# Optimization experiments

Hardware: AMD Instinct MI355X
Metric: run time of the kernel (lower is better)

## Reference

```python
import jax, jax.numpy as jnp
import numpy as np

S = 7          # number of slots
B = 8192       # batch
D = 1024       # input_dim
E = 256        # slot_embedding_dim
H = 512        # rnn_hidden_dim
SH = 256       # slot_hidden_dim
V = 100        # labels per slot (uniform)


def _lstm_cell(x, h, c, W_ih, W_hh, b_ih, b_hh):
    # PyTorch LSTMCell: gates ordered i, f, g, o
    gates = x @ W_ih.T + b_ih + h @ W_hh.T + b_hh
    i, f, g, o = jnp.split(gates, 4, axis=-1)
    i = jax.nn.sigmoid(i); f = jax.nn.sigmoid(f)
    g = jnp.tanh(g); o = jax.nn.sigmoid(o)
    c_new = f * c + i * g
    h_new = o * jnp.tanh(c_new)
    return h_new, c_new


def setup_inputs() -> dict:
    key = jax.random.key(0)
    ks = jax.random.split(key, 24)
    sc = 0.05
    D0 = D + E  # layer-0 input size
    inp = {
        'inputs': jax.random.normal(ks[0], (B, D), jnp.float32),
        'labels': jax.random.randint(ks[1], (S - 1, B), 0, V),
        'start': jax.random.normal(ks[2], (E,), jnp.float32),
        'emb': jax.random.normal(ks[3], (S - 1, V, E), jnp.float32) * sc,
        # layer 0 (input size D0)
        'W_ih0': jax.random.normal(ks[4], (S, 4 * H, D0), jnp.float32) * sc,
        'W_hh0': jax.random.normal(ks[5], (S, 4 * H, H), jnp.float32) * sc,
        'b_ih0': jax.random.normal(ks[6], (S, 4 * H), jnp.float32) * sc,
        'b_hh0': jax.random.normal(ks[7], (S, 4 * H), jnp.float32) * sc,
        'hwN_W0': jax.random.normal(ks[8], (S, H, D0 + H), jnp.float32) * sc,
        'hwN_b0': jax.random.normal(ks[9], (S, H), jnp.float32) * sc,
        'hwL_W0': jax.random.normal(ks[10], (S, H, D0), jnp.float32) * sc,
        # layer 1 (input size H)
        'W_ih1': jax.random.normal(ks[11], (S, 4 * H, H), jnp.float32) * sc,
        'W_hh1': jax.random.normal(ks[12], (S, 4 * H, H), jnp.float32) * sc,
        'b_ih1': jax.random.normal(ks[13], (S, 4 * H), jnp.float32) * sc,
        'b_hh1': jax.random.normal(ks[14], (S, 4 * H), jnp.float32) * sc,
        'hwN_W1': jax.random.normal(ks[15], (S, H, H + H), jnp.float32) * sc,
        'hwN_b1': jax.random.normal(ks[16], (S, H), jnp.float32) * sc,
        'hwL_W1': jax.random.normal(ks[17], (S, H, H), jnp.float32) * sc,
        # slot hidden + classifier
        'sh_W': jax.random.normal(ks[18], (S, SH, H), jnp.float32) * sc,
        'sh_b': jax.random.normal(ks[19], (S, SH), jnp.float32) * sc,
        'pred_W': jax.random.normal(ks[20], (S, V, SH), jnp.float32) * sc,
        'pred_b': jax.random.normal(ks[21], (S, V), jnp.float32) * sc,
    }
    return inp


def reference(inputs, labels, start, emb,
              W_ih0, W_hh0, b_ih0, b_hh0, hwN_W0, hwN_b0, hwL_W0,
              W_ih1, W_hh1, b_ih1, b_hh1, hwN_W1, hwN_b1, hwL_W1,
              sh_W, sh_b, pred_W, pred_b):
    bsz = inputs.shape[0]
    cur_emb = jnp.broadcast_to(start[None, :], (bsz, E))
    h0 = jnp.zeros((bsz, H), inputs.dtype); c0 = jnp.zeros((bsz, H), inputs.dtype)
    h1 = jnp.zeros((bsz, H), inputs.dtype); c1 = jnp.zeros((bsz, H), inputs.dtype)
    logits_all = []
    for i in range(S):  # slots are a short, structurally distinct recurrence
        x = jnp.concatenate([inputs, cur_emb], axis=-1)  # [B, D+E]
        # layer 0
        h0, c0 = _lstm_cell(x, h0, c0, W_ih0[i], W_hh0[i], b_ih0[i], b_hh0[i])
        gate = jax.nn.sigmoid(jnp.concatenate([x, h0], -1) @ hwN_W0[i].T + hwN_b0[i])
        cur = gate * h0 + (1.0 - gate) * (x @ hwL_W0[i].T)
        # layer 1
        h1, c1 = _lstm_cell(cur, h1, c1, W_ih1[i], W_hh1[i], b_ih1[i], b_hh1[i])
        gate1 = jax.nn.sigmoid(jnp.concatenate([cur, h1], -1) @ hwN_W1[i].T + hwN_b1[i])
        # (highway output of last layer feeds nothing further for this slot)
        _ = gate1 * h1 + (1.0 - gate1) * (cur @ hwL_W1[i].T)
        hidden = jax.nn.relu(h1 @ sh_W[i].T + sh_b[i])     # [B, SH]
        logits_all.append(hidden @ pred_W[i].T + pred_b[i])  # [B, V]
        if i < S - 1:
            cur_emb = emb[i][labels[i]]  # teacher-forced embedding lookup
    return jnp.stack(logits_all, axis=0)  # [S, B, V]
```

## Files before the change

### kernel.cpp

```cpp
#include <hip/hip_runtime.h>

#define SLOTS 7
#define BATCH 8192

typedef __attribute__((ext_vector_type(8))) __bf16 bf16x8;
typedef __attribute__((ext_vector_type(4))) float f32x4;

__device__ __forceinline__ void gl_lds16(const __bf16* g, __bf16* l) {
  __builtin_amdgcn_global_load_lds(
      (const __attribute__((address_space(1))) void*)g,
      (__attribute__((address_space(3))) void*)l, 16, 0, 0);
}

__device__ __forceinline__ float sigmoidf_(float x) {
  return 1.f / (1.f + __expf(-x));
}
__device__ __forceinline__ float tanhf_(float x) {
  float xc = fminf(fmaxf(x, -15.f), 15.f);
  float e = __expf(2.f * xc);
  return (e - 1.f) / (e + 1.f);
}

#define VMW(n) asm volatile("s_waitcnt vmcnt(" #n ")" ::: "memory")
#define BARF()                       \
  __builtin_amdgcn_s_barrier();      \
  asm volatile("" ::: "memory")

__global__ void __launch_bounds__(512, 2)
gemm8p(const __bf16* __restrict__ A, int lda,
       const __bf16* __restrict__ Bw, int ldb,
       const float* __restrict__ b_ih, const float* __restrict__ b_hh,
       float* __restrict__ cst, __bf16* __restrict__ hout, int hld, int hoff,
       int N, int NT) {
  extern __shared__ __bf16 lds[];
#define LDSH(b, s) (lds + (((b) << 2) + (s)) * 8192)
  const int tid = threadIdx.x;
  const int w = tid >> 6, lane = tid & 63;
  const int wr = w >> 2, wc = w & 3;
  const int ln = lane & 15, lh = lane >> 4;
  const int nbx = N >> 8;
  const int NB = gridDim.x;
  const int bid = blockIdx.x;
  const int wg = (bid & 7) * (NB >> 3) + (bid >> 3);
  const int bx = wg % nbx, by = wg / nbx;
  const int blockM = by << 8, blockN = bx << 8;

  f32x4 acc[8][4];
#pragma unroll
  for (int i = 0; i < 8; ++i)
#pragma unroll
    for (int j = 0; j < 4; ++j) acc[i][j] = (f32x4){0.f, 0.f, 0.f, 0.f};

  auto stage = [&](int nb, int s, int kt) {
    const __bf16* base = (s & 1) ? Bw : A;
    const int ld = (s & 1) ? ldb : lda;
    const int rb = (s & 1) ? blockN : blockM;
    const int kh = s >> 1;
#pragma unroll
    for (int j = 0; j < 2; ++j) {
      const int c = j * 512 + w * 64 + lane;
      const int row = c >> 2;
      const int blklog = (c & 3) ^ ((c >> 3) & 3);
      const __bf16* src =
          base + (size_t)(rb + row) * ld + kt * 64 + kh * 32 + blklog * 8;
      gl_lds16(src, LDSH(nb, s) + j * 4096 + w * 512);
    }
  };

  bf16x8 a[8], b0[2], b1[2];
  const int swz = ((lh ^ ((ln >> 1) & 3)) << 3);

#define RDA(slot)                                                            \
  {                                                                          \
    const __bf16* ap = LDSH(buf, slot);                                      \
    _Pragma("unroll") for (int mi = 0; mi < 8; ++mi) a[mi] =                 \
        *(const bf16x8*)&ap[(wr * 128 + mi * 16 + ln) * 32 + swz];           \
  }
#define RDB(slot)                                                            \
  {                                                                          \
    const __bf16* bp = LDSH(buf, slot);                                      \
    _Pragma("unroll") for (int ni = 0; ni < 2; ++ni) {                       \
      b0[ni] = *(const bf16x8*)&bp[(wc * 64 + ni * 16 + ln) * 32 + swz];     \
      b1[ni] = *(const bf16x8*)&bp[(wc * 64 + 32 + ni * 16 + ln) * 32 + swz];\
    }                                                                        \
  }
#define MFMAC(bp, nh)                                                        \
  __builtin_amdgcn_s_setprio(1);                                             \
  _Pragma("unroll") for (int mi = 0; mi < 8; ++mi)                           \
      _Pragma("unroll") for (int ni = 0; ni < 2; ++ni)                       \
          acc[mi][(nh)*2 + ni] = __builtin_amdgcn_mfma_f32_16x16x32_bf16(    \
              a[mi], bp[ni], acc[mi][(nh)*2 + ni], 0, 0, 0);                 \
  __builtin_amdgcn_s_setprio(0);

#pragma unroll
  for (int s4 = 0; s4 < 4; ++s4) stage(0, s4, 0);
  VMW(0);
  BARF();

  int buf = 0;
  for (int t = 0; t < NT; ++t) {
    const int nb = buf ^ 1;
    const bool hn = (t + 1 < NT);
    RDA(0); RDB(1);
    if (hn) { stage(nb, 0, t + 1); stage(nb, 1, t + 1); }
    MFMAC(b0, 0); MFMAC(b1, 1);
    RDA(2); RDB(3);
    if (hn) { stage(nb, 2, t + 1); stage(nb, 3, t + 1); }
    MFMAC(b0, 0); MFMAC(b1, 1);
    VMW(0);
    BARF();
    buf = nb;
  }
#undef RDA
#undef RDB
#undef MFMAC
#undef LDSH

  const int row0 = blockM + wr * 128 + (lh << 2);
  const int h = (((blockN >> 6) + wc) << 4) + ln;
  const float bs0 = b_ih[h] + b_hh[h];
  const float bs1 = b_ih[512 + h] + b_hh[512 + h];
  const float bs2 = b_ih[1024 + h] + b_hh[1024 + h];
  const float bs3 = b_ih[1536 + h] + b_hh[1536 + h];
#pragma unroll
  for (int mi = 0; mi < 8; ++mi)
#pragma unroll
    for (int r = 0; r < 4; ++r) {
      const int row = row0 + mi * 16 + r;
      float gi = sigmoidf_(acc[mi][0][r] + bs0);
      float gf = sigmoidf_(acc[mi][1][r] + bs1);
      float gg = tanhf_(acc[mi][2][r] + bs2);
      float go = sigmoidf_(acc[mi][3][r] + bs3);
      const size_t ci = (size_t)row * 512 + h;
      float cn = gf * cst[ci] + gi * gg;
      cst[ci] = cn;
      hout[(size_t)row * hld + hoff + h] = (__bf16)(go * tanhf_(cn));
    }
}

template <int MODE>
__global__ void __launch_bounds__(256)
gemm_bt(const __bf16* __restrict__ A, int lda,
        const __bf16* __restrict__ Bw, int ldb,
        void* __restrict__ Cout, int ldc,
        const float* __restrict__ bias,
        const float* __restrict__ auxr,
        __bf16* __restrict__ hout, int hld, int hoff,
        const __bf16* __restrict__ hsrc,
        int M, int N, int K, int Nreal) {
  __shared__ __align__(16) __bf16 As[2][128 * 32];
  __shared__ __align__(16) __bf16 Bs[2][128 * 32];
  const int w = threadIdx.x >> 6;
  const int lane = threadIdx.x & 63;
  const int wr = w >> 1, wc = w & 1;
  const int rowBase = blockIdx.y << 7;
  const int colBase = blockIdx.x << 7;
  const int sr = lane >> 2;
  const int sc = (lane & 3) << 3;

  f32x4 acc[4][4];
#pragma unroll
  for (int i = 0; i < 4; ++i)
#pragma unroll
    for (int j = 0; j < 4; ++j) acc[i][j] = (f32x4){0.f, 0.f, 0.f, 0.f};

  const int nsteps = K >> 5;

#define STAGE(bi, k0)                                                           \
  {                                                                             \
    const __bf16* ga = A + (size_t)(rowBase + (w << 5) + sr) * lda + (k0) + sc; \
    gl_lds16(ga, &As[(bi)][(w << 5) * 32]);                                     \
    gl_lds16(ga + (size_t)16 * lda, &As[(bi)][((w << 5) + 16) * 32]);           \
    const __bf16* gb = Bw + (size_t)(colBase + (w << 5) + sr) * ldb + (k0) + sc;\
    gl_lds16(gb, &Bs[(bi)][(w << 5) * 32]);                                     \
    gl_lds16(gb + (size_t)16 * ldb, &Bs[(bi)][((w << 5) + 16) * 32]);           \
  }

  STAGE(0, 0);
  __syncthreads();
  int buf = 0;
  const int ln = lane & 15;
  const int kg = (lane >> 4) << 3;
  for (int t = 0; t < nsteps; ++t) {
    if (t + 1 < nsteps) STAGE(buf ^ 1, (t + 1) << 5);
    bf16x8 av[4], bv[4];
#pragma unroll
    for (int i = 0; i < 4; ++i)
      av[i] = *(const bf16x8*)&As[buf][((wr << 6) + (i << 4) + ln) * 32 + kg];
#pragma unroll
    for (int i = 0; i < 4; ++i)
      bv[i] = *(const bf16x8*)&Bs[buf][((wc << 6) + (i << 4) + ln) * 32 + kg];
#pragma unroll
    for (int mi = 0; mi < 4; ++mi)
#pragma unroll
      for (int ni = 0; ni < 4; ++ni)
        acc[mi][ni] = __builtin_amdgcn_mfma_f32_16x16x32_bf16(
            av[mi], bv[ni], acc[mi][ni], 0, 0, 0);
    __syncthreads();
    buf ^= 1;
  }
#undef STAGE

  const int lh = lane >> 4;
  const int row0 = rowBase + (wr << 6) + (lh << 2);
  const int col0 = colBase + (wc << 6) + ln;

  if (MODE == 0) {
    float* C = (float*)Cout;
#pragma unroll
    for (int mi = 0; mi < 4; ++mi)
#pragma unroll
      for (int ni = 0; ni < 4; ++ni) {
        const int col = col0 + (ni << 4);
#pragma unroll
        for (int r = 0; r < 4; ++r)
          C[(size_t)(row0 + (mi << 4) + r) * ldc + col] = acc[mi][ni][r];
      }
  } else if (MODE == 1) {
    __bf16* C = (__bf16*)Cout;
#pragma unroll
    for (int mi = 0; mi < 4; ++mi)
#pragma unroll
      for (int ni = 0; ni < 4; ++ni) {
        const int col = col0 + (ni << 4);
        const float b = bias[col];
#pragma unroll
        for (int r = 0; r < 4; ++r) {
          float v = fmaxf(acc[mi][ni][r] + b, 0.f);
          C[(size_t)(row0 + (mi << 4) + r) * ldc + col] = (__bf16)v;
        }
      }
  } else if (MODE == 2) {
    float* C = (float*)Cout;
#pragma unroll
    for (int mi = 0; mi < 4; ++mi)
#pragma unroll
      for (int ni = 0; ni < 4; ++ni) {
        const int col = col0 + (ni << 4);
        if (col < Nreal) {
          const float b = bias[col];
#pragma unroll
          for (int r = 0; r < 4; ++r)
            C[(size_t)(row0 + (mi << 4) + r) * ldc + col] = acc[mi][ni][r] + b;
        }
      }
  } else if (MODE == 6) {
    __bf16* C = (__bf16*)Cout;
#pragma unroll
    for (int mi = 0; mi < 4; ++mi)
#pragma unroll
      for (int ni = 0; ni < 4; ++ni) {
        const int col = col0 + (ni << 4);
#pragma unroll
        for (int r = 0; r < 4; ++r) {
          const int row = row0 + (mi << 4) + r;
          float xp = auxr[(size_t)row * 1024 + col];
          float hwl = auxr[(size_t)row * 1024 + 512 + col];
          float gn = sigmoidf_(acc[mi][ni][r] + xp + bias[col]);
          float hn = (float)hsrc[(size_t)row * 512 + col];
          C[(size_t)row * ldc + col] = (__bf16)(gn * hn + (1.f - gn) * hwl);
          hout[(size_t)row * hld + hoff + col] = (__bf16)hn;
        }
      }
  }
}

__global__ void pack_w(const float* __restrict__ src, __bf16* __restrict__ dst,
                       int cols, int rows_s, int cols_s,
                       int sLd, int dLd, long dOff, int total) {
  int idx = blockIdx.x * 256 + threadIdx.x;
  if (idx >= total) return;
  int r = idx / cols;
  int c = idx - r * cols;
  float v = (r < rows_s && c < cols_s) ? src[(long)r * sLd + c] : 0.f;
  dst[dOff + (long)r * dLd + c] = (__bf16)v;
}

__global__ void pack_perm(const float* __restrict__ src, __bf16* __restrict__ dst,
                          int cols, int sLd, int dLd, long dColOff, int total) {
  int idx = blockIdx.x * 256 + threadIdx.x;
  if (idx >= total) return;
  int r = idx / cols;
  int c = idx - r * cols;
  int srcr = (((r >> 4) & 3) << 9) + ((r >> 6) << 4) + (r & 15);
  dst[(long)r * dLd + dColOff + c] = (__bf16)src[(long)srcr * sLd + c];
}

__global__ void conv_inputs(const float* __restrict__ in, __bf16* __restrict__ xh) {
  int idx = blockIdx.x * 256 + threadIdx.x;
  int b = idx >> 10, c = idx & 1023;
  xh[(size_t)b * 1792 + c] = (__bf16)in[idx];
}

__global__ void set_start(const float* __restrict__ start, __bf16* __restrict__ xh) {
  int idx = blockIdx.x * 256 + threadIdx.x;
  int b = idx >> 8, e = idx & 255;
  xh[(size_t)b * 1792 + 1024 + e] = (__bf16)start[e];
}

__global__ void emb_gather(const float* __restrict__ emb, const int* __restrict__ labels,
                           __bf16* __restrict__ xh) {
  int idx = blockIdx.x * 256 + threadIdx.x;
  int b = idx >> 8, e = idx & 255;
  int lab = labels[b];
  xh[(size_t)b * 1792 + 1024 + e] = (__bf16)emb[(size_t)lab * 256 + e];
}

__global__ void zero_states(__bf16* __restrict__ xh, __bf16* __restrict__ xh1A) {
  int idx = blockIdx.x * 256 + threadIdx.x;
  int b = idx >> 9, h = idx & 511;
  xh[(size_t)b * 1792 + 1280 + h] = (__bf16)0.f;
  xh1A[(size_t)b * 1024 + 512 + h] = (__bf16)0.f;
}

extern "C" void kernel_launch(void* const* d_in, const int* in_sizes, int n_in,
                              void* d_out, int out_size, void* d_ws, size_t ws_size,
                              hipStream_t stream) {
  const float* inputs = (const float*)d_in[0];
  const int* labels = (const int*)d_in[1];
  const float* start = (const float*)d_in[2];
  const float* emb = (const float*)d_in[3];
  const float* W_ih0 = (const float*)d_in[4];
  const float* W_hh0 = (const float*)d_in[5];
  const float* b_ih0 = (const float*)d_in[6];
  const float* b_hh0 = (const float*)d_in[7];
  const float* hwN_W0 = (const float*)d_in[8];
  const float* hwN_b0 = (const float*)d_in[9];
  const float* hwL_W0 = (const float*)d_in[10];
  const float* W_ih1 = (const float*)d_in[11];
  const float* W_hh1 = (const float*)d_in[12];
  const float* b_ih1 = (const float*)d_in[13];
  const float* b_hh1 = (const float*)d_in[14];
  const float* sh_W = (const float*)d_in[18];
  const float* sh_b = (const float*)d_in[19];
  const float* pred_W = (const float*)d_in[20];
  const float* pred_b = (const float*)d_in[21];
  float* out = (float*)d_out;

  char* p = (char*)d_ws;
  size_t off = 0;
  auto alloc = [&](size_t bytes) {
    void* r = p + off;
    off += (bytes + 255) & ~(size_t)255;
    return r;
  };
  __bf16* WA = (__bf16*)alloc((size_t)2048 * 1792 * 2);
  __bf16* WX = (__bf16*)alloc((size_t)1024 * 1280 * 2);
  __bf16* WH = (__bf16*)alloc((size_t)512 * 512 * 2);
  __bf16* WB = (__bf16*)alloc((size_t)2048 * 1024 * 2);
  __bf16* WS = (__bf16*)alloc((size_t)256 * 512 * 2);
  __bf16* WP = (__bf16*)alloc((size_t)128 * 256 * 2);
  __bf16* xh = (__bf16*)alloc((size_t)BATCH * 1792 * 2);
  __bf16* xh1A = (__bf16*)alloc((size_t)BATCH * 1024 * 2);
  __bf16* xh1B = (__bf16*)alloc((size_t)BATCH * 1024 * 2);
  __bf16* h0new = (__bf16*)alloc((size_t)BATCH * 512 * 2);
  float* ghw = (float*)alloc((size_t)BATCH * 1024 * 4);
  float* c0 = (float*)alloc((size_t)BATCH * 512 * 4);
  float* c1 = (float*)alloc((size_t)BATCH * 512 * 4);
  __bf16* hidden = (__bf16*)ghw;
  (void)ws_size; (void)in_sizes; (void)n_in; (void)out_size;

  hipMemsetAsync(c0, 0, (size_t)BATCH * 512 * 4, stream);
  hipMemsetAsync(c1, 0, (size_t)BATCH * 512 * 4, stream);
  zero_states<<<BATCH * 512 / 256, 256, 0, stream>>>(xh, xh1A);
  conv_inputs<<<BATCH * 1024 / 256, 256, 0, stream>>>(inputs, xh);
  set_start<<<BATCH * 256 / 256, 256, 0, stream>>>(start, xh);

  const dim3 blk(256);
  for (int s = 0; s < SLOTS; ++s) {
    __bf16* xcur = (s & 1) ? xh1B : xh1A;
    __bf16* xnext = (s & 1) ? xh1A : xh1B;
    {
      int t;
      t = 2048 * 1280;
      pack_perm<<<(t + 255) / 256, blk, 0, stream>>>(
          W_ih0 + (size_t)s * 2048 * 1280, WA, 1280, 1280, 1792, 0, t);
      t = 2048 * 512;
      pack_perm<<<(t + 255) / 256, blk, 0, stream>>>(
          W_hh0 + (size_t)s * 2048 * 512, WA, 512, 512, 1792, 1280, t);
      t = 512 * 1280;
      pack_w<<<(t + 255) / 256, blk, 0, stream>>>(
          hwN_W0 + (size_t)s * 512 * 1792, WX, 1280, 512, 1280, 1792, 1280, 0, t);
      pack_w<<<(t + 255) / 256, blk, 0, stream>>>(
          hwL_W0 + (size_t)s * 512 * 1280, WX, 1280, 512, 1280, 1280, 1280,
          (long)512 * 1280, t);
      t = 512 * 512;
      pack_w<<<(t + 255) / 256, blk, 0, stream>>>(
          hwN_W0 + (size_t)s * 512 * 1792 + 1280, WH, 512, 512, 512, 1792, 512, 0, t);
      t = 2048 * 512;
      pack_perm<<<(t + 255) / 256, blk, 0, stream>>>(
          W_ih1 + (size_t)s * 2048 * 512, WB, 512, 512, 1024, 0, t);
      pack_perm<<<(t + 255) / 256, blk, 0, stream>>>(
          W_hh1 + (size_t)s * 2048 * 512, WB, 512, 512, 1024, 512, t);
      t = 256 * 512;
      pack_w<<<(t + 255) / 256, blk, 0, stream>>>(
          sh_W + (size_t)s * 256 * 512, WS, 512, 256, 512, 512, 512, 0, t);
      t = 128 * 256;
      pack_w<<<(t + 255) / 256, blk, 0, stream>>>(
          pred_W + (size_t)s * 100 * 256, WP, 256, 100, 256, 256, 256, 0, t);
    }

    gemm_bt<0><<<dim3(8, 64), blk, 0, stream>>>(
        xh, 1792, WX, 1280, ghw, 1024, nullptr,
        nullptr, nullptr, 0, 0, nullptr, BATCH, 1024, 1280, 1024);
    gemm8p<<<256, 512, 131072, stream>>>(
        xh, 1792, WA, 1792, b_ih0 + s * 2048, b_hh0 + s * 2048,
        c0, h0new, 512, 0, 2048, 28);
    gemm_bt<6><<<dim3(4, 64), blk, 0, stream>>>(
        h0new, 512, WH, 512, xcur, 1024, hwN_b0 + s * 512,
        ghw, xh, 1792, 1280, h0new, BATCH, 512, 512, 512);
    if (s < SLOTS - 1)
      emb_gather<<<BATCH * 256 / 256, blk, 0, stream>>>(
          emb + (size_t)s * 100 * 256, labels + (size_t)s * BATCH, xh);
    gemm8p<<<256, 512, 131072, stream>>>(
        xcur, 1024, WB, 1024, b_ih1 + s * 2048, b_hh1 + s * 2048,
        c1, xnext, 1024, 512, 2048, 16);
    gemm_bt<1><<<dim3(2, 64), blk, 0, stream>>>(
        xnext + 512, 1024, WS, 512, hidden, 256, sh_b + s * 256,
        nullptr, nullptr, 0, 0, nullptr, BATCH, 256, 512, 256);
    gemm_bt<2><<<dim3(1, 64), blk, 0, stream>>>(
        hidden, 256, WP, 256, out + (size_t)s * BATCH * 100, 100,
        pred_b + s * 100, nullptr, nullptr, 0, 0, nullptr, BATCH, 128, 256, 100);
  }
}
```

Measured before the change: 1.655 ms.

## Merge per-slot weight packing kernels into one launch; issue prefetch earlier

Nine separate weight pack/permute launches per slot are replaced by a single pack_all kernel that dispatches on a flattened index range, cutting launch count and tail gaps. Separately, the gemm8p main loop now issues all four next-tile global-to-LDS stages before reading the current tile and running the MFMAs, rather than interleaving them, so loads start earlier. The earlier prefetch may change memory-pipe contention with the LDS reads, and the merged pack kernel adds branch divergence only at segment boundaries.

```diff
diff --git a/kernel.cpp b/kernel.cpp
--- a/kernel.cpp
+++ b/kernel.cpp
@@ -101,11 +101,13 @@
   for (int t = 0; t < NT; ++t) {
     const int nb = buf ^ 1;
     const bool hn = (t + 1 < NT);
+    if (hn) {
+      stage(nb, 0, t + 1); stage(nb, 1, t + 1);
+      stage(nb, 2, t + 1); stage(nb, 3, t + 1);
+    }
     RDA(0); RDB(1);
-    if (hn) { stage(nb, 0, t + 1); stage(nb, 1, t + 1); }
     MFMAC(b0, 0); MFMAC(b1, 1);
     RDA(2); RDB(3);
-    if (hn) { stage(nb, 2, t + 1); stage(nb, 3, t + 1); }
     MFMAC(b0, 0); MFMAC(b1, 1);
     VMW(0);
     BARF();
@@ -265,25 +267,57 @@
   }
 }
 
-__global__ void pack_w(const float* __restrict__ src, __bf16* __restrict__ dst,
-                       int cols, int rows_s, int cols_s,
-                       int sLd, int dLd, long dOff, int total) {
-  int idx = blockIdx.x * 256 + threadIdx.x;
-  if (idx >= total) return;
-  int r = idx / cols;
-  int c = idx - r * cols;
-  float v = (r < rows_s && c < cols_s) ? src[(long)r * sLd + c] : 0.f;
-  dst[dOff + (long)r * dLd + c] = (__bf16)v;
-}
-
-__global__ void pack_perm(const float* __restrict__ src, __bf16* __restrict__ dst,
-                          int cols, int sLd, int dLd, long dColOff, int total) {
-  int idx = blockIdx.x * 256 + threadIdx.x;
-  if (idx >= total) return;
-  int r = idx / cols;
-  int c = idx - r * cols;
-  int srcr = (((r >> 4) & 3) << 9) + ((r >> 6) << 4) + (r & 15);
-  dst[(long)r * dLd + dColOff + c] = (__bf16)src[(long)srcr * sLd + c];
+#define PR0 2621440
+#define PR1 3670016
+#define PR2 4325376
+#define PR3 4980736
+#define PR4 5242880
+#define PR5 6291456
+#define PR6 7340032
+#define PR7 7471104
+#define PR8 7503872
+__global__ void pack_all(const float* __restrict__ W_ih0, const float* __restrict__ W_hh0,
+                         const float* __restrict__ hwN_W0, const float* __restrict__ hwL_W0,
+                         const float* __restrict__ W_ih1, const float* __restrict__ W_hh1,
+                         const float* __restrict__ sh_W, const float* __restrict__ pred_W,
+                         __bf16* __restrict__ WA, __bf16* __restrict__ WX,
+                         __bf16* __restrict__ WH, __bf16* __restrict__ WB,
+                         __bf16* __restrict__ WS, __bf16* __restrict__ WP, int s) {
+  const int idx = blockIdx.x * 256 + threadIdx.x;
+  if (idx >= PR8) return;
+  if (idx < PR0) {
+    int i = idx, r = i / 1280, c = i - r * 1280;
+    int sr = (((r >> 4) & 3) << 9) + ((r >> 6) << 4) + (r & 15);
+    WA[(long)r * 1792 + c] = (__bf16)W_ih0[(size_t)s * 2048 * 1280 + (long)sr * 1280 + c];
+  } else if (idx < PR1) {
+    int i = idx - PR0, r = i >> 9, c = i & 511;
+    int sr = (((r >> 4) & 3) << 9) + ((r >> 6) << 4) + (r & 15);
+    WA[(long)r * 1792 + 1280 + c] = (__bf16)W_hh0[(size_t)s * 2048 * 512 + (long)sr * 512 + c];
+  } else if (idx < PR2) {
+    int i = idx - PR1, r = i / 1280, c = i - r * 1280;
+    WX[(long)r * 1280 + c] = (__bf16)hwN_W0[(size_t)s * 512 * 1792 + (long)r * 1792 + c];
+  } else if (idx < PR3) {
+    int i = idx - PR2, r = i / 1280, c = i - r * 1280;
+    WX[(long)(512 + r) * 1280 + c] = (__bf16)hwL_W0[(size_t)s * 512 * 1280 + (long)r * 1280 + c];
+  } else if (idx < PR4) {
+    int i = idx - PR3, r = i >> 9, c = i & 511;
+    WH[(long)r * 512 + c] = (__bf16)hwN_W0[(size_t)s * 512 * 1792 + (long)r * 1792 + 1280 + c];
+  } else if (idx < PR5) {
+    int i = idx - PR4, r = i >> 9, c = i & 511;
+    int sr = (((r >> 4) & 3) << 9) + ((r >> 6) << 4) + (r & 15);
+    WB[(long)r * 1024 + c] = (__bf16)W_ih1[(size_t)s * 2048 * 512 + (long)sr * 512 + c];
+  } else if (idx < PR6) {
+    int i = idx - PR5, r = i >> 9, c = i & 511;
+    int sr = (((r >> 4) & 3) << 9) + ((r >> 6) << 4) + (r & 15);
+    WB[(long)r * 1024 + 512 + c] = (__bf16)W_hh1[(size_t)s * 2048 * 512 + (long)sr * 512 + c];
+  } else if (idx < PR7) {
+    int i = idx - PR6, r = i >> 9, c = i & 511;
+    WS[(long)r * 512 + c] = (__bf16)sh_W[(size_t)s * 256 * 512 + (long)r * 512 + c];
+  } else {
+    int i = idx - PR7, r = i >> 8, c = i & 255;
+    float v = (r < 100) ? pred_W[(size_t)s * 100 * 256 + (long)r * 256 + c] : 0.f;
+    WP[(long)r * 256 + c] = (__bf16)v;
+  }
 }
 
 __global__ void conv_inputs(const float* __restrict__ in, __bf16* __restrict__ xh) {
@@ -370,35 +404,9 @@
   for (int s = 0; s < SLOTS; ++s) {
     __bf16* xcur = (s & 1) ? xh1B : xh1A;
     __bf16* xnext = (s & 1) ? xh1A : xh1B;
-    {
-      int t;
-      t = 2048 * 1280;
-      pack_perm<<<(t + 255) / 256, blk, 0, stream>>>(
-          W_ih0 + (size_t)s * 2048 * 1280, WA, 1280, 1280, 1792, 0, t);
-      t = 2048 * 512;
-      pack_perm<<<(t + 255) / 256, blk, 0, stream>>>(
-          W_hh0 + (size_t)s * 2048 * 512, WA, 512, 512, 1792, 1280, t);
-      t = 512 * 1280;
-      pack_w<<<(t + 255) / 256, blk, 0, stream>>>(
-          hwN_W0 + (size_t)s * 512 * 1792, WX, 1280, 512, 1280, 1792, 1280, 0, t);
-      pack_w<<<(t + 255) / 256, blk, 0, stream>>>(
-          hwL_W0 + (size_t)s * 512 * 1280, WX, 1280, 512, 1280, 1280, 1280,
-          (long)512 * 1280, t);
-      t = 512 * 512;
-      pack_w<<<(t + 255) / 256, blk, 0, stream>>>(
-          hwN_W0 + (size_t)s * 512 * 1792 + 1280, WH, 512, 512, 512, 1792, 512, 0, t);
-      t = 2048 * 512;
-      pack_perm<<<(t + 255) / 256, blk, 0, stream>>>(
-          W_ih1 + (size_t)s * 2048 * 512, WB, 512, 512, 1024, 0, t);
-      pack_perm<<<(t + 255) / 256, blk, 0, stream>>>(
-          W_hh1 + (size_t)s * 2048 * 512, WB, 512, 512, 1024, 512, t);
-      t = 256 * 512;
-      pack_w<<<(t + 255) / 256, blk, 0, stream>>>(
-          sh_W + (size_t)s * 256 * 512, WS, 512, 256, 512, 512, 512, 0, t);
-      t = 128 * 256;
-      pack_w<<<(t + 255) / 256, blk, 0, stream>>>(
-          pred_W + (size_t)s * 100 * 256, WP, 256, 100, 256, 256, 256, 0, t);
-    }
+    pack_all<<<(PR8 + 255) / 256, blk, 0, stream>>>(
+        W_ih0, W_hh0, hwN_W0, hwL_W0, W_ih1, W_hh1, sh_W, pred_W,
+        WA, WX, WH, WB, WS, WP, s);
 
     gemm_bt<0><<<dim3(8, 64), blk, 0, stream>>>(
         xh, 1792, WX, 1280, ghw, 1024, nullptr,
```

After: 1.540 ms. 1.07x faster.
